# Optimization experiments

Hardware: AMD Instinct MI355X
Metric: run time of the kernel (lower is better)

The kernel has to match this reference:

```python
import jax, jax.numpy as jnp
import numpy as np

B, S, D, H = 4, 1024, 1024, 16
E = 8                 # num_experts
FF1 = 4096            # d_hidden * expansion_factor * 2 (swiglu in)
FF2 = 2048            # d_hidden * expansion_factor (swiglu out / linear2 in)
TEMP = 0.5            # gating temperature
RMS_EPS_GATE = float(np.finfo(np.float32).eps)  # torch RMSNorm default eps
NORM_EPS = 1e-8       # layer_norm_eps


def setup_inputs() -> dict:
    key = jax.random.key(0)
    ks = jax.random.split(key, 8)
    s = 0.02
    return {
        "x": jax.random.normal(ks[0], (B, S, D), jnp.float32),
        "w_qkv": jax.random.normal(ks[1], (3 * D, D), jnp.float32) * s,
        "w_out": jax.random.normal(ks[2], (D, D), jnp.float32) * s,
        "norm1_w": jnp.ones((D,), jnp.float32),
        "norm2_w": jnp.ones((D,), jnp.float32),
        "gate_w": jax.random.normal(ks[3], (E, D), jnp.float32) * s,
        "gate_b": jnp.zeros((E,), jnp.float32),
        "gate_rms_w": jnp.ones((E,), jnp.float32),
        "w1": jax.random.normal(ks[4], (E, D, FF1), jnp.float32) * s,
        "w2": jax.random.normal(ks[5], (E, FF2, D), jnp.float32) * s,
    }


def _rmsnorm(x, w, eps):
    return x * w * jax.lax.rsqrt(jnp.mean(x * x, axis=-1, keepdims=True) + eps)


def _attn(h, w_qkv, w_out):
    qkv = h @ w_qkv.T                              # [B,S,3D]
    q, k, v = jnp.split(qkv, 3, axis=-1)
    dh = D // H
    q = q.reshape(B, S, H, dh)
    k = k.reshape(B, S, H, dh)
    v = v.reshape(B, S, H, dh)
    scores = jnp.einsum("bqhd,bkhd->bhqk", q, k) / jnp.sqrt(jnp.float32(dh))
    p = jax.nn.softmax(scores, axis=-1)
    o = jnp.einsum("bhqk,bkhd->bqhd", p, v).reshape(B, S, D)
    return o @ w_out.T


def _moe(h, gate_w, gate_b, gate_rms_w, w1, w2):
    xf = h.reshape(-1, D)                          # [N,D]
    logits = _rmsnorm(xf @ gate_w.T + gate_b, gate_rms_w, RMS_EPS_GATE)
    gates = jax.nn.softmax(logits / TEMP, axis=-1)  # [N,E]
    top_g, _ = jax.lax.top_k(gates, 1)              # top_k = 1
    # capacity dispatch mask degenerates to all-ones (capacity >= 1), so
    # normalized gate = g / (g + 1e-6)
    g = top_g[:, 0] / (top_g[:, 0] + 1e-6)          # [N]
    h1 = jnp.einsum("nd,edf->nef", xf, w1)          # [N,E,FF1]
    a, b = jnp.split(h1, 2, axis=-1)                # SwiGLU
    act = a * jax.nn.silu(b)                        # [N,E,FF2]
    outs = jnp.einsum("nef,efd->ned", act, w2)      # [N,E,D]
    # gate broadcasts over the expert axis (as in the original code)
    comb = outs.sum(axis=1) * g[:, None]
    return comb.reshape(h.shape)


def reference(x, w_qkv, w_out, norm1_w, norm2_w, gate_w, gate_b, gate_rms_w, w1, w2):
    # pre-norm transformer block, eval mode (no dropout / gating noise)
    x = x + _attn(_rmsnorm(x, norm1_w, NORM_EPS), w_qkv, w_out)
    x = x + _moe(_rmsnorm(x, norm2_w, NORM_EPS), gate_w, gate_b, gate_rms_w, w1, w2)
    return x
```

## Files before the change

kernel.cpp:

```cpp
#include <hip/hip_runtime.h>
#include <hip/hip_bf16.h>
#include <math.h>

typedef __bf16 bf16_t;
typedef __bf16 bf16x8 __attribute__((ext_vector_type(8)));
typedef float f32x4 __attribute__((ext_vector_type(4)));

typedef const __attribute__((address_space(1))) void* gptr_t;
typedef __attribute__((address_space(3))) void* lptr_t;

#define MFMA16(a, b, c) __builtin_amdgcn_mfma_f32_16x16x32_bf16((a), (b), (c), 0, 0, 0)
#define BAR() __builtin_amdgcn_s_barrier()
#define WAIT_LGKM()                                        \
  do {                                                     \
    asm volatile("s_waitcnt lgkmcnt(0)" ::: "memory");     \
    __builtin_amdgcn_sched_barrier(0);                     \
  } while (0)
#define WAIT_VM8()                                         \
  do {                                                     \
    asm volatile("s_waitcnt vmcnt(8)" ::: "memory");       \
    __builtin_amdgcn_sched_barrier(0);                     \
  } while (0)
#define WAIT_VM0()                                         \
  do {                                                     \
    asm volatile("s_waitcnt vmcnt(0)" ::: "memory");       \
    __builtin_amdgcn_sched_barrier(0);                     \
  } while (0)

__device__ __forceinline__ void gload_lds16(const bf16_t* g, bf16_t* l) {
  __builtin_amdgcn_global_load_lds((gptr_t)g, (lptr_t)l, 16, 0, 0);
}

__global__ __launch_bounds__(256) void conv_kernel(const float* __restrict__ in,
                                                   bf16_t* __restrict__ out, int n4) {
  int i = blockIdx.x * 256 + threadIdx.x;
  if (i >= n4) return;
  float4 v = ((const float4*)in)[i];
  bf16_t* o = out + (size_t)i * 4;
  o[0] = (bf16_t)v.x; o[1] = (bf16_t)v.y; o[2] = (bf16_t)v.z; o[3] = (bf16_t)v.w;
}

__global__ __launch_bounds__(256) void transp_w1(const float* __restrict__ in,
                                                 bf16_t* __restrict__ out) {
  __shared__ float tile[32][33];
  const float* ip = in + (size_t)blockIdx.z * 1024 * 4096;
  bf16_t* op = out + (size_t)blockIdx.z * 4096 * 1024;
  int tx = threadIdx.x, ty = threadIdx.y;
  int r0 = blockIdx.y * 32, c0 = blockIdx.x * 32;
#pragma unroll
  for (int i = 0; i < 32; i += 8)
    tile[ty + i][tx] = ip[(size_t)(r0 + ty + i) * 4096 + c0 + tx];
  __syncthreads();
#pragma unroll
  for (int i = 0; i < 32; i += 8) {
    int c = c0 + ty + i;
    int p = (c < 2048) ? ((c >> 5) * 64 + (c & 31))
                       : (((c - 2048) >> 5) * 64 + 32 + ((c - 2048) & 31));
    op[(size_t)p * 1024 + r0 + tx] = (bf16_t)tile[tx][ty + i];
  }
}

__global__ __launch_bounds__(256) void transp_w2(const float* __restrict__ in,
                                                 bf16_t* __restrict__ out) {
  __shared__ float tile[32][33];
  const float* ip = in + (size_t)blockIdx.z * 2048 * 1024;
  int tx = threadIdx.x, ty = threadIdx.y;
  int r0 = blockIdx.y * 32, c0 = blockIdx.x * 32;
#pragma unroll
  for (int i = 0; i < 32; i += 8)
    tile[ty + i][tx] = ip[(size_t)(r0 + ty + i) * 1024 + c0 + tx];
  __syncthreads();
#pragma unroll
  for (int i = 0; i < 32; i += 8)
    out[(size_t)(c0 + ty + i) * 16384 + blockIdx.z * 2048 + r0 + tx] = (bf16_t)tile[tx][ty + i];
}

__global__ __launch_bounds__(256) void rmsnorm_kernel(const float* __restrict__ x,
                                                      const float* __restrict__ w,
                                                      bf16_t* __restrict__ out, float eps) {
  int row = blockIdx.x;
  int t = threadIdx.x;
  const float4* xr = (const float4*)(x + (size_t)row * 1024);
  float4 v = xr[t];
  float ss = v.x * v.x + v.y * v.y + v.z * v.z + v.w * v.w;
#pragma unroll
  for (int off = 1; off < 64; off <<= 1) ss += __shfl_xor(ss, off, 64);
  __shared__ float red[4];
  int wave = t >> 6, lane = t & 63;
  if (lane == 0) red[wave] = ss;
  __syncthreads();
  ss = red[0] + red[1] + red[2] + red[3];
  float inv = rsqrtf(ss * (1.0f / 1024.0f) + eps);
  float4 wv = ((const float4*)w)[t];
  bf16_t* o = out + (size_t)row * 1024 + t * 4;
  o[0] = (bf16_t)(v.x * wv.x * inv);
  o[1] = (bf16_t)(v.y * wv.y * inv);
  o[2] = (bf16_t)(v.z * wv.z * inv);
  o[3] = (bf16_t)(v.w * wv.w * inv);
}

template <int EPI>
__global__ __launch_bounds__(512, 2) void gemm256(const bf16_t* __restrict__ A,
                                                  const bf16_t* __restrict__ Bt,
                                                  void* __restrict__ C,
                                                  const float* __restrict__ resid,
                                                  int M, int N, int K, int lda, int ldb) {
  __shared__ bf16_t As[2][256 * 64];
  __shared__ bf16_t Bs[2][256 * 64];
  const int tid = threadIdx.x;
  const int wave = tid >> 6, lane = tid & 63;

  const int gx = gridDim.x, gy = gridDim.y;
  int nwg = gx * gy * gridDim.z;
  int lin = blockIdx.x + gx * (blockIdx.y + gy * blockIdx.z);
  int wid = ((nwg & 7) == 0) ? ((lin & 7) * (nwg >> 3) + (lin >> 3)) : lin;
  const int bx = wid % gx;
  const int by = (wid / gx) % gy;
  const int bz = wid / (gx * gy);

  const int m0 = by * 256, n0 = bx * 256;
  const int wr = (wave >> 2) * 128, wc = (wave & 3) * 64;
  const int fr = lane & 15, fq = lane >> 4;

  if (EPI == 4) Bt += (size_t)bz * 4096 * 1024;
  if (EPI == 5) {
    A += (size_t)bz * K;
    Bt += (size_t)bz * K;
  }

  const int srw = lane >> 3;
  const int sgc = (lane & 7) ^ srw;
  const bf16_t* aBase = A + (size_t)(m0 + wave * 8 + srw) * lda + sgc * 8;
  const bf16_t* bBase = Bt + (size_t)(n0 + wave * 8 + srw) * ldb + sgc * 8;

  auto stageA = [&](bf16_t* buf, int kt) {
#pragma unroll
    for (int i = 0; i < 4; ++i) {
      int r = i * 64;
      gload_lds16(aBase + (size_t)r * lda + kt * 64, &buf[(r + wave * 8) * 64]);
    }
  };
  auto stageB = [&](bf16_t* buf, int kt) {
#pragma unroll
    for (int i = 0; i < 4; ++i) {
      int r = i * 64;
      gload_lds16(bBase + (size_t)r * ldb + kt * 64, &buf[(r + wave * 8) * 64]);
    }
  };

  f32x4 acc[8][4] = {};
  bf16x8 a_[4][2], b_[4][2];

  auto readA = [&](int b, int mh) {
#pragma unroll
    for (int q = 0; q < 4; ++q)
#pragma unroll
      for (int ks = 0; ks < 2; ++ks) {
        int r = wr + mh * 64 + q * 16 + fr;
        a_[q][ks] = *(const bf16x8*)&As[b][r * 64 + (((fq + ks * 4) ^ (fr & 7)) << 3)];
      }
  };
  auto readB = [&](int b, int nh) {
#pragma unroll
    for (int q = 0; q < 2; ++q)
#pragma unroll
      for (int ks = 0; ks < 2; ++ks) {
        int r = wc + nh * 32 + q * 16 + fr;
        b_[nh * 2 + q][ks] = *(const bf16x8*)&Bs[b][r * 64 + (((fq + ks * 4) ^ (fr & 7)) << 3)];
      }
  };
  auto mfma16x = [&](int mh, int nh) {
    __builtin_amdgcn_s_setprio(1);
#pragma unroll
    for (int q = 0; q < 4; ++q)
#pragma unroll
      for (int n = 0; n < 2; ++n)
#pragma unroll
        for (int ks = 0; ks < 2; ++ks)
          acc[mh * 4 + q][nh * 2 + n] =
              MFMA16(a_[q][ks], b_[nh * 2 + n][ks], acc[mh * 4 + q][nh * 2 + n]);
    __builtin_amdgcn_s_setprio(0);
  };

  const int NKT = K >> 6;
  stageB(Bs[0], 0);
  stageA(As[0], 0);
  stageB(Bs[1], 1);
  stageA(As[1], 1);
  WAIT_VM8();
  BAR();

  for (int it = 0; it < (NKT >> 1) - 1; ++it) {
    const int t2 = 2 * it + 2, t3 = 2 * it + 3;
    readA(0, 0); readB(0, 0);
    BAR(); WAIT_LGKM(); mfma16x(0, 0); BAR();
    readB(0, 1);
    BAR(); WAIT_LGKM(); mfma16x(0, 1); BAR();
    readA(0, 1);
    stageB(Bs[0], t2);
    BAR(); WAIT_LGKM(); mfma16x(1, 0); BAR();
    stageA(As[0], t2);
    BAR(); mfma16x(1, 1);
    WAIT_VM8();
    BAR();
    readA(1, 0); readB(1, 0);
    BAR(); WAIT_LGKM(); mfma16x(0, 0); BAR();
    readB(1, 1);
    BAR(); WAIT_LGKM(); mfma16x(0, 1); BAR();
    readA(1, 1);
    stageB(Bs[1], t3);
    BAR(); WAIT_LGKM(); mfma16x(1, 0); BAR();
    stageA(As[1], t3);
    BAR(); mfma16x(1, 1);
    WAIT_VM8();
    BAR();
  }

  {
    readA(0, 0); readB(0, 0);
    BAR(); WAIT_LGKM(); mfma16x(0, 0); BAR();
    readB(0, 1);
    BAR(); WAIT_LGKM(); mfma16x(0, 1); BAR();
    readA(0, 1);
    BAR(); WAIT_LGKM(); mfma16x(1, 0); BAR();
    BAR(); mfma16x(1, 1);
    WAIT_VM0();
    BAR();
    readA(1, 0); readB(1, 0);
    BAR(); WAIT_LGKM(); mfma16x(0, 0); BAR();
    readB(1, 1);
    BAR(); WAIT_LGKM(); mfma16x(0, 1); BAR();
    readA(1, 1);
    BAR(); WAIT_LGKM(); mfma16x(1, 0); BAR();
    mfma16x(1, 1);
  }

  if (EPI == 4) {
    bf16_t* act = (bf16_t*)C;
    int strip = (n0 >> 6) + (wave & 3);
#pragma unroll
    for (int mq = 0; mq < 8; ++mq)
#pragma unroll
      for (int n = 0; n < 2; ++n)
#pragma unroll
        for (int j = 0; j < 4; ++j) {
          size_t row = (size_t)(m0 + wr + mq * 16 + fq * 4 + j);
          size_t col = (size_t)bz * 2048 + strip * 32 + n * 16 + fr;
          float a = acc[mq][n][j], b = acc[mq][n + 2][j];
          act[row * 16384 + col] = (bf16_t)(a * (b / (1.0f + __expf(-b))));
        }
    return;
  }
#pragma unroll
  for (int mq = 0; mq < 8; ++mq)
#pragma unroll
    for (int n = 0; n < 4; ++n)
#pragma unroll
      for (int j = 0; j < 4; ++j) {
        size_t row = (size_t)(m0 + wr + mq * 16 + fq * 4 + j);
        size_t col = (size_t)(n0 + wc + n * 16 + fr);
        float v = acc[mq][n][j];
        if (EPI == 0)
          ((bf16_t*)C)[row * N + col] = (bf16_t)v;
        else if (EPI == 1)
          ((float*)C)[row * N + col] = resid[row * N + col] + v;
        else if (EPI == 5)
          ((float*)C + (size_t)bz * M * N)[row * N + col] = v;
      }
}

__global__ __launch_bounds__(256) void attn_kernel(const bf16_t* __restrict__ qkv,
                                                   bf16_t* __restrict__ o) {
  const int S = 1024, LD = 3072;
  int qt = blockIdx.x, bh = blockIdx.y;
  int b = bh >> 4, h = bh & 15;
  int tid = threadIdx.x, wave = tid >> 6, lane = tid & 63;
  int fr = lane & 15, fq = lane >> 4, kg = fq * 8;
  int q0 = qt * 64 + wave * 16;
  const bf16_t* qb = qkv + (size_t)b * S * LD + h * 64;
  const bf16_t* kb = qb + 1024;
  const bf16_t* vb = qb + 2048;

  __shared__ bf16_t Ks[64 * 64];
  __shared__ bf16_t Vt[64 * 64];
  __shared__ bf16_t Ps[4][16 * 72];

  bf16x8 qf0 = *(const bf16x8*)&qb[(size_t)(q0 + fr) * LD + kg];
  bf16x8 qf1 = *(const bf16x8*)&qb[(size_t)(q0 + fr) * LD + 32 + kg];

  f32x4 acc[4] = {};
  float mrow[4] = {-1e30f, -1e30f, -1e30f, -1e30f};
  float ssum[4] = {0.f, 0.f, 0.f, 0.f};

  for (int k0 = 0; k0 < S; k0 += 64) {
#pragma unroll
    for (int cc = 0; cc < 2; ++cc) {
      int c = tid + cc * 256;
      int r = c >> 3, ch = c & 7;
      *(bf16x8*)&Ks[r * 64 + ((ch ^ (r & 7)) << 3)] =
          *(const bf16x8*)&kb[(size_t)(k0 + r) * LD + ch * 8];
      bf16x8 vv = *(const bf16x8*)&vb[(size_t)(k0 + r) * LD + ch * 8];
#pragma unroll
      for (int i = 0; i < 8; ++i) {
        int d = ch * 8 + i;
        int cs = ((r >> 3) ^ (d >> 3) ^ (d & 7)) & 7;
        Vt[d * 64 + cs * 8 + (r & 7)] = vv[i];
      }
    }
    __syncthreads();

    f32x4 s[4];
#pragma unroll
    for (int kc = 0; kc < 4; ++kc) {
      int row = kc * 16 + fr, sw = row & 7;
      bf16x8 kf0 = *(const bf16x8*)&Ks[row * 64 + ((fq ^ sw) << 3)];
      bf16x8 kf1 = *(const bf16x8*)&Ks[row * 64 + (((4 + fq) ^ sw) << 3)];
      f32x4 z = {};
      z = MFMA16(qf0, kf0, z);
      z = MFMA16(qf1, kf1, z);
      s[kc] = z * 0.125f;
    }
    float pmax[4], psum[4], scl[4];
#pragma unroll
    for (int j = 0; j < 4; ++j)
      pmax[j] = fmaxf(fmaxf(s[0][j], s[1][j]), fmaxf(s[2][j], s[3][j]));
#pragma unroll
    for (int off = 1; off < 16; off <<= 1)
#pragma unroll
      for (int j = 0; j < 4; ++j) pmax[j] = fmaxf(pmax[j], __shfl_xor(pmax[j], off, 64));
#pragma unroll
    for (int j = 0; j < 4; ++j) {
      float nm = fmaxf(mrow[j], pmax[j]);
      scl[j] = __expf(mrow[j] - nm);
      mrow[j] = nm;
      psum[j] = 0.f;
    }
#pragma unroll
    for (int kc = 0; kc < 4; ++kc)
#pragma unroll
      for (int j = 0; j < 4; ++j) {
        float p = __expf(s[kc][j] - mrow[j]);
        psum[j] += p;
        Ps[wave][(fq * 4 + j) * 72 + kc * 16 + fr] = (bf16_t)p;
      }
#pragma unroll
    for (int off = 1; off < 16; off <<= 1)
#pragma unroll
      for (int j = 0; j < 4; ++j) psum[j] += __shfl_xor(psum[j], off, 64);
#pragma unroll
    for (int j = 0; j < 4; ++j) ssum[j] = ssum[j] * scl[j] + psum[j];
#pragma unroll
    for (int n = 0; n < 4; ++n)
#pragma unroll
      for (int j = 0; j < 4; ++j) acc[n][j] *= scl[j];
    asm volatile("s_waitcnt lgkmcnt(0)" ::: "memory");
    bf16x8 pa[2];
#pragma unroll
    for (int ks = 0; ks < 2; ++ks) pa[ks] = *(const bf16x8*)&Ps[wave][fr * 72 + ks * 32 + kg];
#pragma unroll
    for (int n = 0; n < 4; ++n) {
      int d = n * 16 + fr;
      int swd = ((d >> 3) ^ (d & 7)) & 7;
#pragma unroll
      for (int ks = 0; ks < 2; ++ks) {
        bf16x8 vbf = *(const bf16x8*)&Vt[d * 64 + (((ks * 4 + fq) ^ swd) << 3)];
        acc[n] = MFMA16(pa[ks], vbf, acc[n]);
      }
    }
    __syncthreads();
  }
#pragma unroll
  for (int n = 0; n < 4; ++n)
#pragma unroll
    for (int j = 0; j < 4; ++j) {
      size_t row = (size_t)b * S + q0 + fq * 4 + j;
      o[row * 1024 + h * 64 + n * 16 + fr] = (bf16_t)(acc[n][j] / ssum[j]);
    }
}

__global__ __launch_bounds__(256) void gate_kernel(const bf16_t* __restrict__ hn,
                                                   const float* __restrict__ gw,
                                                   const float* __restrict__ gb,
                                                   const float* __restrict__ grms,
                                                   float* __restrict__ g) {
  int n = blockIdx.x * 4 + (threadIdx.x >> 6);
  int lane = threadIdx.x & 63;
  const bf16_t* xr = hn + (size_t)n * 1024;
  float acc[8] = {};
  for (int i = lane; i < 1024; i += 64) {
    float xv = (float)xr[i];
#pragma unroll
    for (int e = 0; e < 8; ++e) acc[e] += xv * gw[e * 1024 + i];
  }
#pragma unroll
  for (int e = 0; e < 8; ++e)
    for (int off = 1; off < 64; off <<= 1) acc[e] += __shfl_xor(acc[e], off, 64);
  float l[8], ms = 0.f;
#pragma unroll
  for (int e = 0; e < 8; ++e) {
    l[e] = acc[e] + gb[e];
    ms += l[e] * l[e];
  }
  float inv = rsqrtf(ms * 0.125f + 1.1920928955078125e-07f);
  float mx = -1e30f;
#pragma unroll
  for (int e = 0; e < 8; ++e) {
    l[e] = l[e] * inv * grms[e] * 2.0f;
    mx = fmaxf(mx, l[e]);
  }
  float s = 0.f;
#pragma unroll
  for (int e = 0; e < 8; ++e) s += __expf(l[e] - mx);
  float t = 1.0f / s;
  if (lane == 0) g[n] = t / (t + 1e-6f);
}

__global__ __launch_bounds__(256) void combine8(const float* __restrict__ moep,
                                                const float* __restrict__ x1,
                                                const float* __restrict__ g,
                                                float* __restrict__ out, int Mc) {
  size_t i4 = (size_t)blockIdx.x * 256 + threadIdx.x;
  size_t row = i4 >> 8;
  size_t stride4 = (size_t)Mc * 256;
  float4 s = {0.f, 0.f, 0.f, 0.f};
#pragma unroll
  for (int z = 0; z < 8; ++z) {
    float4 v = ((const float4*)moep)[z * stride4 + i4];
    s.x += v.x; s.y += v.y; s.z += v.z; s.w += v.w;
  }
  float gv = g[row];
  float4 xv = ((const float4*)x1)[i4];
  float4 r;
  r.x = xv.x + s.x * gv;
  r.y = xv.y + s.y * gv;
  r.z = xv.z + s.z * gv;
  r.w = xv.w + s.w * gv;
  ((float4*)out)[i4] = r;
}

extern "C" void kernel_launch(void* const* d_in, const int* in_sizes, int n_in,
                              void* d_out, int out_size, void* d_ws, size_t ws_size,
                              hipStream_t stream) {
  const float* x = (const float*)d_in[0];
  const float* w_qkv = (const float*)d_in[1];
  const float* w_out = (const float*)d_in[2];
  const float* norm1_w = (const float*)d_in[3];
  const float* norm2_w = (const float*)d_in[4];
  const float* gate_w = (const float*)d_in[5];
  const float* gate_b = (const float*)d_in[6];
  const float* gate_rms = (const float*)d_in[7];
  const float* w1 = (const float*)d_in[8];
  const float* w2 = (const float*)d_in[9];
  float* out = (float*)d_out;

  const size_t baseB = (8ull * 4096 * 1024 + 1024ull * 16384 + 3072ull * 1024 +
                        1024ull * 1024 + 4096ull * 1024) * 2 +
                       4096ull * 1024 * 4 + 4096 * 4;
  int cc = 4;
  if (ws_size >= baseB + 4096ull * 16384 * 2 + 8ull * 4096 * 1024 * 4)
    cc = 1;
  else if (ws_size >= baseB + 2048ull * 16384 * 2 + 8ull * 2048 * 1024 * 4)
    cc = 2;
  const int Mc = 4096 / cc;

  char* ws = (char*)d_ws;
  size_t off = 0;
  auto alloc = [&](size_t bytes) {
    char* p = ws + off;
    off += bytes;
    return p;
  };
  bf16_t* w1t = (bf16_t*)alloc(8ull * 4096 * 1024 * 2);
  bf16_t* w2t = (bf16_t*)alloc(1024ull * 16384 * 2);
  bf16_t* wqkvb = (bf16_t*)alloc(3072ull * 1024 * 2);
  bf16_t* woutb = (bf16_t*)alloc(1024ull * 1024 * 2);
  bf16_t* hn = (bf16_t*)alloc(4096ull * 1024 * 2);
  float* x1 = (float*)alloc(4096ull * 1024 * 4);
  float* gbuf = (float*)alloc(4096ull * 4);
  bf16_t* act = (bf16_t*)alloc((size_t)Mc * 16384 * 2);
  float* moep = (float*)alloc(8ull * Mc * 1024 * 4);
  bf16_t* qkvb = (bf16_t*)act;
  bf16_t* attno = (bf16_t*)moep;

  conv_kernel<<<3072, 256, 0, stream>>>(w_qkv, wqkvb, 3072 * 1024 / 4);
  conv_kernel<<<1024, 256, 0, stream>>>(w_out, woutb, 1024 * 1024 / 4);
  transp_w1<<<dim3(128, 32, 8), dim3(32, 8), 0, stream>>>(w1, w1t);
  transp_w2<<<dim3(32, 64, 8), dim3(32, 8), 0, stream>>>(w2, w2t);

  rmsnorm_kernel<<<4096, 256, 0, stream>>>(x, norm1_w, hn, 1e-8f);
  gemm256<0><<<dim3(12, 16), 512, 0, stream>>>(hn, wqkvb, qkvb, nullptr, 4096, 3072, 1024,
                                               1024, 1024);
  attn_kernel<<<dim3(16, 64), 256, 0, stream>>>(qkvb, attno);
  gemm256<1><<<dim3(4, 16), 512, 0, stream>>>(attno, woutb, x1, x, 4096, 1024, 1024, 1024,
                                              1024);

  rmsnorm_kernel<<<4096, 256, 0, stream>>>(x1, norm2_w, hn, 1e-8f);
  gate_kernel<<<1024, 256, 0, stream>>>(hn, gate_w, gate_b, gate_rms, gbuf);
  for (int c = 0; c < cc; ++c) {
    gemm256<4><<<dim3(16, Mc / 256, 8), 512, 0, stream>>>(
        hn + (size_t)c * Mc * 1024, w1t, act, nullptr, Mc, 4096, 1024, 1024, 1024);
    gemm256<5><<<dim3(4, Mc / 256, 8), 512, 0, stream>>>(
        act, w2t, moep, nullptr, Mc, 1024, 2048, 16384, 16384);
    combine8<<<Mc, 256, 0, stream>>>(moep, x1 + (size_t)c * Mc * 1024, gbuf + (size_t)c * Mc,
                                     out + (size_t)c * Mc * 1024, Mc);
  }
}
```

Baseline: 651.6 us.

## Software-pipeline LDS reads in GEMM main loop and halve split-K partials for MoE down-proj

Restructures the GEMM K-loop so each MFMA phase is immediately followed by the next LDS fragment reads and global staging, with one barrier per phase instead of two, and prefetches the first fragments before the loop. Global-load waits move to vmcnt(4) at the stage points. The second MoE GEMM now splits K into 4 slices of 4096 (two experts each) instead of 8 slices of 2048, halving the fp32 partial buffer and the reads in the combine kernel. This trades fewer partial writes and less combine traffic for fewer blocks in the down-projection grid, and the reordered waits and barriers risk LDS hazards if any are missed.

```diff
diff --git a/kernel.cpp b/kernel.cpp
--- a/kernel.cpp
+++ b/kernel.cpp
@@ -14,6 +14,11 @@
 #define WAIT_LGKM()                                        \
   do {                                                     \
     asm volatile("s_waitcnt lgkmcnt(0)" ::: "memory");     \
+    __builtin_amdgcn_sched_barrier(0);                     \
+  } while (0)
+#define WAIT_VM4()                                         \
+  do {                                                     \
+    asm volatile("s_waitcnt vmcnt(4)" ::: "memory");       \
     __builtin_amdgcn_sched_barrier(0);                     \
   } while (0)
 #define WAIT_VM8()                                         \
@@ -189,51 +194,29 @@
   stageA(As[1], 1);
   WAIT_VM8();
   BAR();
+  readA(0, 0);
+  readB(0, 0);
 
   for (int it = 0; it < (NKT >> 1) - 1; ++it) {
     const int t2 = 2 * it + 2, t3 = 2 * it + 3;
-    readA(0, 0); readB(0, 0);
-    BAR(); WAIT_LGKM(); mfma16x(0, 0); BAR();
-    readB(0, 1);
-    BAR(); WAIT_LGKM(); mfma16x(0, 1); BAR();
-    readA(0, 1);
-    stageB(Bs[0], t2);
-    BAR(); WAIT_LGKM(); mfma16x(1, 0); BAR();
-    stageA(As[0], t2);
-    BAR(); mfma16x(1, 1);
-    WAIT_VM8();
-    BAR();
-    readA(1, 0); readB(1, 0);
-    BAR(); WAIT_LGKM(); mfma16x(0, 0); BAR();
-    readB(1, 1);
-    BAR(); WAIT_LGKM(); mfma16x(0, 1); BAR();
-    readA(1, 1);
-    stageB(Bs[1], t3);
-    BAR(); WAIT_LGKM(); mfma16x(1, 0); BAR();
-    stageA(As[1], t3);
-    BAR(); mfma16x(1, 1);
-    WAIT_VM8();
-    BAR();
-  }
-
-  {
-    readA(0, 0); readB(0, 0);
-    BAR(); WAIT_LGKM(); mfma16x(0, 0); BAR();
-    readB(0, 1);
-    BAR(); WAIT_LGKM(); mfma16x(0, 1); BAR();
-    readA(0, 1);
-    BAR(); WAIT_LGKM(); mfma16x(1, 0); BAR();
-    BAR(); mfma16x(1, 1);
-    WAIT_VM0();
-    BAR();
-    readA(1, 0); readB(1, 0);
-    BAR(); WAIT_LGKM(); mfma16x(0, 0); BAR();
-    readB(1, 1);
-    BAR(); WAIT_LGKM(); mfma16x(0, 1); BAR();
-    readA(1, 1);
-    BAR(); WAIT_LGKM(); mfma16x(1, 0); BAR();
-    mfma16x(1, 1);
-  }
+    WAIT_LGKM(); mfma16x(0, 0); readB(0, 1); BAR();
+    WAIT_LGKM(); mfma16x(0, 1); readA(0, 1); BAR();
+    WAIT_LGKM(); mfma16x(1, 0); stageB(Bs[0], t2); WAIT_VM4(); BAR();
+    WAIT_LGKM(); mfma16x(1, 1); readA(1, 0); readB(1, 0); stageA(As[0], t2); BAR();
+    WAIT_LGKM(); mfma16x(0, 0); readB(1, 1); BAR();
+    WAIT_LGKM(); mfma16x(0, 1); readA(1, 1); BAR();
+    WAIT_LGKM(); mfma16x(1, 0); stageB(Bs[1], t3); WAIT_VM4(); BAR();
+    WAIT_LGKM(); mfma16x(1, 1); readA(0, 0); readB(0, 0); stageA(As[1], t3); BAR();
+  }
+
+  WAIT_LGKM(); mfma16x(0, 0); readB(0, 1); BAR();
+  WAIT_LGKM(); mfma16x(0, 1); readA(0, 1); BAR();
+  WAIT_LGKM(); mfma16x(1, 0); WAIT_VM0(); BAR();
+  WAIT_LGKM(); mfma16x(1, 1); readA(1, 0); readB(1, 0); BAR();
+  WAIT_LGKM(); mfma16x(0, 0); readB(1, 1); BAR();
+  WAIT_LGKM(); mfma16x(0, 1); readA(1, 1); BAR();
+  WAIT_LGKM(); mfma16x(1, 0); BAR();
+  WAIT_LGKM(); mfma16x(1, 1);
 
   if (EPI == 4) {
     bf16_t* act = (bf16_t*)C;
@@ -415,7 +398,7 @@
   if (lane == 0) g[n] = t / (t + 1e-6f);
 }
 
-__global__ __launch_bounds__(256) void combine8(const float* __restrict__ moep,
+__global__ __launch_bounds__(256) void combine4(const float* __restrict__ moep,
                                                 const float* __restrict__ x1,
                                                 const float* __restrict__ g,
                                                 float* __restrict__ out, int Mc) {
@@ -424,7 +407,7 @@
   size_t stride4 = (size_t)Mc * 256;
   float4 s = {0.f, 0.f, 0.f, 0.f};
 #pragma unroll
-  for (int z = 0; z < 8; ++z) {
+  for (int z = 0; z < 4; ++z) {
     float4 v = ((const float4*)moep)[z * stride4 + i4];
     s.x += v.x; s.y += v.y; s.z += v.z; s.w += v.w;
   }
@@ -457,9 +440,9 @@
                         1024ull * 1024 + 4096ull * 1024) * 2 +
                        4096ull * 1024 * 4 + 4096 * 4;
   int cc = 4;
-  if (ws_size >= baseB + 4096ull * 16384 * 2 + 8ull * 4096 * 1024 * 4)
+  if (ws_size >= baseB + 4096ull * 16384 * 2 + 4ull * 4096 * 1024 * 4)
     cc = 1;
-  else if (ws_size >= baseB + 2048ull * 16384 * 2 + 8ull * 2048 * 1024 * 4)
+  else if (ws_size >= baseB + 2048ull * 16384 * 2 + 4ull * 2048 * 1024 * 4)
     cc = 2;
   const int Mc = 4096 / cc;
 
@@ -478,7 +461,7 @@
   float* x1 = (float*)alloc(4096ull * 1024 * 4);
   float* gbuf = (float*)alloc(4096ull * 4);
   bf16_t* act = (bf16_t*)alloc((size_t)Mc * 16384 * 2);
-  float* moep = (float*)alloc(8ull * Mc * 1024 * 4);
+  float* moep = (float*)alloc(4ull * Mc * 1024 * 4);
   bf16_t* qkvb = (bf16_t*)act;
   bf16_t* attno = (bf16_t*)moep;
 
@@ -499,9 +482,9 @@
   for (int c = 0; c < cc; ++c) {
     gemm256<4><<<dim3(16, Mc / 256, 8), 512, 0, stream>>>(
         hn + (size_t)c * Mc * 1024, w1t, act, nullptr, Mc, 4096, 1024, 1024, 1024);
-    gemm256<5><<<dim3(4, Mc / 256, 8), 512, 0, stream>>>(
-        act, w2t, moep, nullptr, Mc, 1024, 2048, 16384, 16384);
-    combine8<<<Mc, 256, 0, stream>>>(moep, x1 + (size_t)c * Mc * 1024, gbuf + (size_t)c * Mc,
+    gemm256<5><<<dim3(4, Mc / 256, 4), 512, 0, stream>>>(
+        act, w2t, moep, nullptr, Mc, 1024, 4096, 16384, 16384);
+    combine4<<<Mc, 256, 0, stream>>>(moep, x1 + (size_t)c * Mc * 1024, gbuf + (size_t)c * Mc,
                                      out + (size_t)c * Mc * 1024, Mc);
   }
 }
```

Result: faster. 604.9 us (-7.2%).
